# Kernel tuning notes

Hardware: AMD Instinct MI355X
Metric: run time of the kernel (lower is better)

Reference implementation:

```python
import jax, jax.numpy as jnp
import numpy as np

B, S, HID = 2, 2048, 2048
H, KVH, D = 32, 4, 128
EPS = 1e-6
ROPE_THETA = 1e6
INIT = 0.02


def setup_inputs() -> dict:
    key = jax.random.key(0)
    ks = jax.random.split(key, 6)
    hidden_states = jax.random.normal(ks[0], (B, S, HID), jnp.float32)
    q_w = jax.random.normal(ks[1], (HID, H * D), jnp.float32) * INIT
    k_w = jax.random.normal(ks[2], (HID, KVH * D), jnp.float32) * INIT
    v_w = jax.random.normal(ks[3], (HID, KVH * D), jnp.float32) * INIT
    o_w = jax.random.normal(ks[4], (H * D, HID), jnp.float32) * INIT
    q_norm_w = jnp.ones((D,), jnp.float32)
    k_norm_w = jnp.ones((D,), jnp.float32)
    # rotary embeddings, computed once per position (B, S, D)
    pos = jnp.arange(S, dtype=jnp.float32)
    inv_freq = 1.0 / (ROPE_THETA ** (jnp.arange(0, D, 2, dtype=jnp.float32) / D))
    freqs = pos[:, None] * inv_freq[None, :]          # (S, D/2)
    emb = jnp.concatenate([freqs, freqs], axis=-1)    # (S, D)
    cos = jnp.broadcast_to(jnp.cos(emb)[None], (B, S, D))
    sin = jnp.broadcast_to(jnp.sin(emb)[None], (B, S, D))
    # causal mask (is_causal=True, sliding_window=None)
    attn_mask = jnp.tril(jnp.ones((S, S), bool))[None, None]  # (1,1,S,S)
    return {"hidden_states": hidden_states, "cos": cos, "sin": sin,
            "q_w": q_w, "k_w": k_w, "v_w": v_w, "o_w": o_w,
            "q_norm_w": q_norm_w, "k_norm_w": k_norm_w, "attn_mask": attn_mask}


def _rms_norm(x, w):
    xf = x.astype(jnp.float32)
    var = jnp.mean(jax.lax.square(xf), axis=-1, keepdims=True)
    return (w * (xf * jax.lax.rsqrt(var + EPS))).astype(x.dtype)


def _rotate_half(x):
    x1, x2 = jnp.split(x, 2, axis=-1)
    return jnp.concatenate([-x2, x1], axis=-1)


def _apply_rope(q, k, cos, sin):
    # q: (B,H,S,D), k: (B,KVH,S,D); cos/sin: (B,S,D) -> (B,1,S,D)
    cos = cos[:, None]
    sin = sin[:, None]
    q = q * cos + _rotate_half(q) * sin
    k = k * cos + _rotate_half(k) * sin
    return q, k


def reference(hidden_states, cos, sin, q_w, k_w, v_w, o_w, q_norm_w, k_norm_w, attn_mask):
    b, s, _ = hidden_states.shape
    scaling = D ** (-0.5)
    # projections + per-head QK RMSNorm
    q = _rms_norm((hidden_states @ q_w).reshape(b, s, H, D), q_norm_w)
    k = _rms_norm((hidden_states @ k_w).reshape(b, s, KVH, D), k_norm_w)
    v = (hidden_states @ v_w).reshape(b, s, KVH, D)
    q = jnp.transpose(q, (0, 2, 1, 3))   # (b,H,s,D)
    k = jnp.transpose(k, (0, 2, 1, 3))   # (b,KVH,s,D)
    v = jnp.transpose(v, (0, 2, 1, 3))
    q, k = _apply_rope(q, k, cos, sin)
    # GQA: repeat KV heads across groups
    groups = H // KVH
    k = jnp.repeat(k, groups, axis=1)    # (b,H,s,D)
    v = jnp.repeat(v, groups, axis=1)
    # eager softmax attention (fp32 softmax)
    scores = jnp.einsum('bhqd,bhkd->bhqk', q, k).astype(jnp.float32) * scaling
    scores = jnp.where(attn_mask, scores, jnp.float32(-1e30))
    probs = jax.nn.softmax(scores, axis=-1).astype(q.dtype)
    attn = jnp.einsum('bhqk,bhkd->bhqd', probs, v)
    attn = jnp.transpose(attn, (0, 2, 1, 3)).reshape(b, s, H * D)
    return attn @ o_w
```

## Files before the change

### kernel.cpp

```cpp
#include <hip/hip_runtime.h>
#include <hip/hip_bf16.h>

typedef unsigned short u16;
typedef __attribute__((ext_vector_type(4))) float f32x4;
typedef __attribute__((ext_vector_type(16))) float f32x16;
typedef __attribute__((ext_vector_type(8))) short bf16x8;
typedef __attribute__((ext_vector_type(4))) unsigned u32x4;

#define B_ 2
#define S_ 2048
#define HID_ 2048
#define H_ 32
#define KVH_ 4
#define D_ 128
#define M_ 4096
#define NQ_ 4096
#define NKV_ 512

typedef const __attribute__((address_space(1))) void gconst_void;
typedef __attribute__((address_space(3))) void lds_void;

static __device__ __forceinline__ void gload_lds16(const void* g, void* l) {
  __builtin_amdgcn_global_load_lds((gconst_void*)g, (lds_void*)l, 16, 0, 0);
}

#define WAITV(N) asm volatile("s_waitcnt vmcnt(" #N ")" ::: "memory")
#define WAITL0() asm volatile("s_waitcnt lgkmcnt(0)" ::: "memory")
#define SBAR() __builtin_amdgcn_s_barrier()
#define SCHED0() __builtin_amdgcn_sched_barrier(0)
#define CFENCE() asm volatile("" ::: "memory")

static __device__ __forceinline__ u16 f2b(float f) {
  union { float f; unsigned i; } x; x.f = f;
  return (u16)((x.i + 0x7fffu + ((x.i >> 16) & 1u)) >> 16);
}
static __device__ __forceinline__ float b2f(u16 u) {
  union { unsigned i; float f; } x; x.i = ((unsigned)u) << 16;
  return x.f;
}
static __device__ __forceinline__ float max3f(float a, float b, float c) {
  float d;
  asm("v_max3_f32 %0, %1, %2, %3" : "=v"(d) : "v"(a), "v"(b), "v"(c));
  return d;
}

static __device__ __forceinline__ void tr_tile(const float* __restrict__ W,
    u16* __restrict__ Wt, int K, int N, int n0, int k0, u16 (*t)[72]) {
  int tid = threadIdx.x;
  int r = tid >> 4;
  int c4 = (tid & 15) * 4;
#pragma unroll
  for (int i = 0; i < 4; i++) {
    int k = r + i * 16;
    float4 v = *reinterpret_cast<const float4*>(W + (size_t)(k0 + k) * N + n0 + c4);
    t[k][c4 + 0] = f2b(v.x); t[k][c4 + 1] = f2b(v.y);
    t[k][c4 + 2] = f2b(v.z); t[k][c4 + 3] = f2b(v.w);
  }
  __syncthreads();
#pragma unroll
  for (int i = 0; i < 4; i++) {
    int n = r + i * 16;
    ushort4 o;
    o.x = t[c4 + 0][n]; o.y = t[c4 + 1][n]; o.z = t[c4 + 2][n]; o.w = t[c4 + 3][n];
    *reinterpret_cast<ushort4*>(Wt + (size_t)(n0 + n) * K + k0 + c4) = o;
  }
}

__global__ __launch_bounds__(256) void k_prep(const float* __restrict__ hidden, u16* __restrict__ hb,
    const float* __restrict__ qw, u16* __restrict__ qwt,
    const float* __restrict__ kw, u16* __restrict__ kwt,
    const float* __restrict__ vw, u16* __restrict__ vwt,
    const float* __restrict__ ow, u16* __restrict__ owt) {
  __shared__ u16 t[64][72];
  const int bid = blockIdx.x;
  if (bid < 2048) {
    const int n4 = M_ * HID_ / 4;
    int i = bid * 256 + threadIdx.x;
    const int stride = 2048 * 256;
    for (; i < n4; i += stride) {
      float4 v = reinterpret_cast<const float4*>(hidden)[i];
      ushort4 o;
      o.x = f2b(v.x); o.y = f2b(v.y); o.z = f2b(v.z); o.w = f2b(v.w);
      reinterpret_cast<ushort4*>(hb)[i] = o;
    }
  } else if (bid < 4096) {
    int l = bid - 2048;
    tr_tile(qw, qwt, HID_, NQ_, (l & 63) * 64, (l >> 6) * 64, t);
  } else if (bid < 4352) {
    int l = bid - 4096;
    tr_tile(kw, kwt, HID_, NKV_, (l & 7) * 64, (l >> 3) * 64, t);
  } else if (bid < 4608) {
    int l = bid - 4352;
    tr_tile(vw, vwt, HID_, NKV_, (l & 7) * 64, (l >> 3) * 64, t);
  } else {
    int l = bid - 4608;
    tr_tile(ow, owt, NQ_, HID_, (l & 31) * 64, (l >> 5) * 64, t);
  }
}

__device__ __forceinline__ void gemm_core(const u16* __restrict__ A, const u16* __restrict__ Bt,
                                          int K, int m0, int n0,
                                          u16* As, u16* Bs, f32x4 (&acc)[4][4]) {
  const int tid = threadIdx.x;
  const int lane = tid & 63;
  const int wid = tid >> 6;
  const int wr = wid >> 1, wc = wid & 1;
  const int lrow = lane & 15;
  const int hi = lane >> 4;
  const f32x4 zz = {0.f, 0.f, 0.f, 0.f};
#pragma unroll
  for (int i = 0; i < 4; i++)
#pragma unroll
    for (int j = 0; j < 4; j++) acc[i][j] = zz;

  const int srow = tid >> 3;
  const int sc16 = tid & 7;
  const int nk = K >> 6;
  int cur = 0;

#pragma unroll
  for (int rep = 0; rep < 4; rep++) {
    int row = rep * 32 + srow;
    int gcol = ((sc16 ^ (row & 7)) << 3);
    gload_lds16(A + (size_t)(m0 + row) * K + gcol, As + row * 64 + sc16 * 8);
    gload_lds16(Bt + (size_t)(n0 + row) * K + gcol, Bs + row * 64 + sc16 * 8);
  }

  for (int t = 0; t < nk; t++) {
    if (t + 1 < nk) {
      int nxt = cur ^ 1;
      int kb = (t + 1) << 6;
#pragma unroll
      for (int rep = 0; rep < 4; rep++) {
        int row = rep * 32 + srow;
        int gcol = kb + ((sc16 ^ (row & 7)) << 3);
        gload_lds16(A + (size_t)(m0 + row) * K + gcol, As + nxt * 8192 + row * 64 + sc16 * 8);
        gload_lds16(Bt + (size_t)(n0 + row) * K + gcol, Bs + nxt * 8192 + row * 64 + sc16 * 8);
      }
      WAITV(8);
    } else {
      WAITV(0);
    }
    SCHED0(); SBAR(); CFENCE(); SCHED0();

    const u16* Ac = As + cur * 8192;
    const u16* Bc = Bs + cur * 8192;
#pragma unroll
    for (int kc = 0; kc < 2; kc++) {
      bf16x8 af[4], bfr[4];
#pragma unroll
      for (int i = 0; i < 4; i++) {
        int row = wr * 64 + i * 16 + lrow;
        af[i] = *reinterpret_cast<const bf16x8*>(Ac + row * 64 + ((((kc << 2) + hi) ^ (row & 7)) << 3));
      }
#pragma unroll
      for (int j = 0; j < 4; j++) {
        int row = wc * 64 + j * 16 + lrow;
        bfr[j] = *reinterpret_cast<const bf16x8*>(Bc + row * 64 + ((((kc << 2) + hi) ^ (row & 7)) << 3));
      }
#pragma unroll
      for (int i = 0; i < 4; i++)
#pragma unroll
        for (int j = 0; j < 4; j++)
          acc[i][j] = __builtin_amdgcn_mfma_f32_16x16x32_bf16(af[i], bfr[j], acc[i][j], 0, 0, 0);
    }
    SBAR(); SCHED0();
    cur ^= 1;
  }
}

__global__ __launch_bounds__(512, 2) void k_gemm_q8(const u16* __restrict__ A,
    const u16* __restrict__ Bt, u16* __restrict__ qb) {
  __shared__ u16 Ash[2][2][128 * 64];
  __shared__ u16 Bsh[2][2][128 * 64];
  const int bid = blockIdx.x;
  const int wg = (bid & 7) * 32 + (bid >> 3);
  const int mt = wg & 15, nt = wg >> 4;
  const int m0 = mt * 256, n0 = nt * 256;
  const int K = HID_, nk = K >> 6;
  const int tid = threadIdx.x, lane = tid & 63;
  const int wv = tid >> 6, wr = wv >> 2, wc = wv & 3;
  const int lrow = lane & 15, hi4 = lane >> 4;

  const int s0r = tid >> 3, sc = tid & 7;
  const int s1r = (tid + 512) >> 3;

  auto stgA = [&](int h, int t, int d) {
    gload_lds16(A + (size_t)(m0 + h * 128 + s0r) * K + t * 64 + ((sc ^ (s0r & 7)) << 3),
                &Ash[d][h][s0r * 64 + sc * 8]);
    gload_lds16(A + (size_t)(m0 + h * 128 + s1r) * K + t * 64 + ((sc ^ (s1r & 7)) << 3),
                &Ash[d][h][s1r * 64 + sc * 8]);
  };
  auto stgB = [&](int h, int t, int d) {
    gload_lds16(Bt + (size_t)(n0 + h * 128 + s0r) * K + t * 64 + ((sc ^ (s0r & 7)) << 3),
                &Bsh[d][h][s0r * 64 + sc * 8]);
    gload_lds16(Bt + (size_t)(n0 + h * 128 + s1r) * K + t * 64 + ((sc ^ (s1r & 7)) << 3),
                &Bsh[d][h][s1r * 64 + sc * 8]);
  };

  f32x4 acc[8][4];
  const f32x4 zz = {0.f, 0.f, 0.f, 0.f};
#pragma unroll
  for (int f = 0; f < 8; f++)
#pragma unroll
    for (int j = 0; j < 4; j++) acc[f][j] = zz;

  bf16x8 af0[4][2], af1[4][2], bfr[2][2];

  auto lda = [&](bf16x8 (&dst)[4][2], int mh, int d) {
#pragma unroll
    for (int fi = 0; fi < 4; fi++) {
      int row = fi * 32 + wr * 16 + lrow;
#pragma unroll
      for (int kk = 0; kk < 2; kk++)
        dst[fi][kk] = *reinterpret_cast<const bf16x8*>(
            &Ash[d][mh][row * 64 + ((((kk << 2) + hi4) ^ (row & 7)) << 3)]);
    }
  };
  auto ldb = [&](int nh, int d) {
#pragma unroll
    for (int ji = 0; ji < 2; ji++) {
      int row = ji * 64 + wc * 16 + lrow;
#pragma unroll
      for (int kk = 0; kk < 2; kk++)
        bfr[ji][kk] = *reinterpret_cast<const bf16x8*>(
            &Bsh[d][nh][row * 64 + ((((kk << 2) + hi4) ^ (row & 7)) << 3)]);
    }
  };
  auto mq = [&](bf16x8 (&afh)[4][2], int mh, int nh) {
    __builtin_amdgcn_s_setprio(1);
#pragma unroll
    for (int kk = 0; kk < 2; kk++)
#pragma unroll
      for (int fi = 0; fi < 4; fi++)
#pragma unroll
        for (int ji = 0; ji < 2; ji++)
          acc[mh * 4 + fi][nh * 2 + ji] = __builtin_amdgcn_mfma_f32_16x16x32_bf16(
              afh[fi][kk], bfr[ji][kk], acc[mh * 4 + fi][nh * 2 + ji], 0, 0, 0);
    __builtin_amdgcn_s_setprio(0);
  };

  stgA(0, 0, 0); stgA(1, 0, 0); stgB(0, 0, 0); stgB(1, 0, 0);
  WAITV(2); SCHED0();
  SBAR(); SCHED0();

  for (int t = 0; t < nk; t++) {
    const int d = t & 1, nd = d ^ 1;
    const bool pre = (t + 1 < nk);
    lda(af0, 0, d); ldb(0, d);
    if (pre) stgA(0, t + 1, nd);
    SCHED0(); SBAR();
    WAITL0(); SCHED0();
    mq(af0, 0, 0);
    SBAR(); SCHED0();
    lda(af1, 1, d);
    if (pre) stgA(1, t + 1, nd);
    WAITV(4); SCHED0(); SBAR();
    WAITL0(); SCHED0();
    mq(af1, 1, 0);
    SBAR(); SCHED0();
    ldb(1, d);
    if (pre) stgB(0, t + 1, nd);
    SCHED0(); SBAR();
    WAITL0(); SCHED0();
    mq(af1, 1, 1);
    SBAR(); SCHED0();
    if (pre) stgB(1, t + 1, nd);
    WAITV(2); SCHED0(); SBAR();
    mq(af0, 0, 1);
    SBAR(); SCHED0();
  }

  const int lr4 = hi4 * 4, lc = lane & 15;
#pragma unroll
  for (int f = 0; f < 8; f++)
#pragma unroll
    for (int j = 0; j < 4; j++)
#pragma unroll
      for (int rr = 0; rr < 4; rr++) {
        int m = m0 + f * 32 + wr * 16 + lr4 + rr;
        int ncol = n0 + j * 64 + wc * 16 + lc;
        int b = m >> 11, s = m & (S_ - 1);
        int head = ncol >> 7, dd = ncol & 127;
        qb[(((size_t)b * H_ + head) * S_ + s) * D_ + dd] = f2b(acc[f][j][rr]);
      }
}

__global__ __launch_bounds__(256, 2) void k_gemm_kv(const u16* __restrict__ hb,
    const u16* __restrict__ kwt, const u16* __restrict__ vwt,
    u16* __restrict__ kb, u16* __restrict__ vb) {
  __shared__ u16 As[2 * 128 * 64], Bs[2 * 128 * 64];
  const int bid = blockIdx.x;
  const int wg = (bid & 7) * 32 + (bid >> 3);
  const int mt = wg & 31, nt = wg >> 5;
  const bool isv = nt >= 4;
  const int head = isv ? nt - 4 : nt;
  const u16* Bt = isv ? vwt : kwt;
  f32x4 acc[4][4];
  gemm_core(hb, Bt, HID_, mt * 128, head * 128, As, Bs, acc);
  const int lane = threadIdx.x & 63;
  const int wid = threadIdx.x >> 6;
  const int wr = wid >> 1, wc = wid & 1;
  const int lr4 = (lane >> 4) * 4, lc = lane & 15;
#pragma unroll
  for (int i = 0; i < 4; i++)
#pragma unroll
    for (int j = 0; j < 4; j++)
#pragma unroll
      for (int r = 0; r < 4; r++) {
        int m = mt * 128 + wr * 64 + i * 16 + lr4 + r;
        int d = wc * 64 + j * 16 + lc;
        int b = m >> 11, s = m & (S_ - 1);
        u16 val = f2b(acc[i][j][r]);
        if (isv) vb[(((size_t)b * KVH_ + head) * D_ + d) * S_ + s] = val;
        else     kb[(((size_t)b * KVH_ + head) * S_ + s) * D_ + d] = val;
      }
}

__global__ __launch_bounds__(512, 2) void k_gemm_o8(const u16* __restrict__ A,
    const u16* __restrict__ Bt, float* __restrict__ out) {
  __shared__ u16 Ash[2][2][128 * 64];
  __shared__ u16 Bsh[2][128 * 64];
  const int bid = blockIdx.x;
  const int wg = (bid & 7) * 32 + (bid >> 3);
  const int mt = wg & 15, nt = wg >> 4;
  const int m0 = mt * 256, n0 = nt * 128;
  const int K = NQ_, nk = K >> 6;
  const int tid = threadIdx.x, lane = tid & 63;
  const int wv = tid >> 6, wr = wv >> 2, wc = wv & 3;
  const int lrow = lane & 15, hi4 = lane >> 4;

  const int s0r = tid >> 3, sc = tid & 7;
  const int s1r = (tid + 512) >> 3;

  auto stgA = [&](int h, int t, int d) {
    gload_lds16(A + (size_t)(m0 + h * 128 + s0r) * K + t * 64 + ((sc ^ (s0r & 7)) << 3),
                &Ash[d][h][s0r * 64 + sc * 8]);
    gload_lds16(A + (size_t)(m0 + h * 128 + s1r) * K + t * 64 + ((sc ^ (s1r & 7)) << 3),
                &Ash[d][h][s1r * 64 + sc * 8]);
  };
  auto stgB = [&](int t, int d) {
    gload_lds16(Bt + (size_t)(n0 + s0r) * K + t * 64 + ((sc ^ (s0r & 7)) << 3),
                &Bsh[d][s0r * 64 + sc * 8]);
    gload_lds16(Bt + (size_t)(n0 + s1r) * K + t * 64 + ((sc ^ (s1r & 7)) << 3),
                &Bsh[d][s1r * 64 + sc * 8]);
  };

  f32x4 acc[8][2];
  const f32x4 zz = {0.f, 0.f, 0.f, 0.f};
#pragma unroll
  for (int f = 0; f < 8; f++) { acc[f][0] = zz; acc[f][1] = zz; }

  bf16x8 af0[4][2], af1[4][2], bfr[2][2];

  auto lda = [&](bf16x8 (&dst)[4][2], int mh, int d) {
#pragma unroll
    for (int fi = 0; fi < 4; fi++) {
      int row = fi * 32 + wr * 16 + lrow;
#pragma unroll
      for (int kk = 0; kk < 2; kk++)
        dst[fi][kk] = *reinterpret_cast<const bf16x8*>(
            &Ash[d][mh][row * 64 + ((((kk << 2) + hi4) ^ (row & 7)) << 3)]);
    }
  };
  auto ldb = [&](int d) {
#pragma unroll
    for (int ji = 0; ji < 2; ji++) {
      int row = ji * 64 + wc * 16 + lrow;
#pragma unroll
      for (int kk = 0; kk < 2; kk++)
        bfr[ji][kk] = *reinterpret_cast<const bf16x8*>(
            &Bsh[d][row * 64 + ((((kk << 2) + hi4) ^ (row & 7)) << 3)]);
    }
  };
  auto mq = [&](bf16x8 (&afh)[4][2], int mh) {
    __builtin_amdgcn_s_setprio(1);
#pragma unroll
    for (int kk = 0; kk < 2; kk++)
#pragma unroll
      for (int fi = 0; fi < 4; fi++)
#pragma unroll
        for (int ji = 0; ji < 2; ji++)
          acc[mh * 4 + fi][ji] = __builtin_amdgcn_mfma_f32_16x16x32_bf16(
              afh[fi][kk], bfr[ji][kk], acc[mh * 4 + fi][ji], 0, 0, 0);
    __builtin_amdgcn_s_setprio(0);
  };

  stgA(0, 0, 0); stgB(0, 0); stgA(1, 0, 0);
  WAITV(2); SCHED0();
  SBAR(); SCHED0();

  for (int t = 0; t < nk; t++) {
    const int d = t & 1, nd = d ^ 1;
    const bool pre = (t + 1 < nk);
    lda(af0, 0, d); ldb(d);
    if (pre) { stgA(0, t + 1, nd); WAITV(2); } else { WAITV(0); }
    SCHED0(); SBAR();
    WAITL0(); SCHED0();
    mq(af0, 0);
    SBAR(); SCHED0();
    lda(af1, 1, d);
    if (pre) { stgB(t + 1, nd); stgA(1, t + 1, nd); WAITV(4); }
    SCHED0(); SBAR();
    WAITL0(); SCHED0();
    mq(af1, 1);
    if (pre) WAITV(2);
    SCHED0(); SBAR(); SCHED0();
  }

  const int lr4 = hi4 * 4, lc = lane & 15;
#pragma unroll
  for (int f = 0; f < 8; f++)
#pragma unroll
    for (int j = 0; j < 2; j++)
#pragma unroll
      for (int rr = 0; rr < 4; rr++) {
        int m = m0 + f * 32 + wr * 16 + lr4 + rr;
        int n = n0 + j * 64 + wc * 16 + lc;
        out[(size_t)m * HID_ + n] = acc[f][j][rr];
      }
}

__global__ __launch_bounds__(256) void k_norm_rope(u16* __restrict__ qb, u16* __restrict__ kb,
    const float* __restrict__ cosp, const float* __restrict__ sinp,
    const float* __restrict__ qnw, const float* __restrict__ knw) {
  int row = blockIdx.x * 4 + (threadIdx.x >> 6);
  int lane = threadIdx.x & 63;
  const int QROWS = B_ * H_ * S_;
  u16* ptr; const float* nw; int b, s; float os;
  if (row < QROWS) {
    ptr = qb + (size_t)row * D_; nw = qnw;
    s = row & (S_ - 1); b = row / (H_ * S_);
    os = 0.08838834764831845f * 1.44269504088896340f;
  } else {
    int r2 = row - QROWS;
    ptr = kb + (size_t)r2 * D_; nw = knw;
    s = r2 & (S_ - 1); b = r2 / (KVH_ * S_);
    os = 1.0f;
  }
  int d = lane * 2;
  float x0 = b2f(ptr[d]), x1 = b2f(ptr[d + 1]);
  float ss = x0 * x0 + x1 * x1;
#pragma unroll
  for (int m = 1; m < 64; m <<= 1) ss += __shfl_xor(ss, m);
  float inv = rsqrtf(ss * (1.0f / 128.0f) + 1e-6f) * os;
  x0 = x0 * inv * nw[d]; x1 = x1 * inv * nw[d + 1];
  float p0 = __shfl_xor(x0, 32), p1 = __shfl_xor(x1, 32);
  float r0 = (lane < 32) ? -p0 : p0;
  float r1 = (lane < 32) ? -p1 : p1;
  const float* cp = cosp + ((size_t)b * S_ + s) * D_;
  const float* sp = sinp + ((size_t)b * S_ + s) * D_;
  ptr[d]     = f2b(x0 * cp[d]     + r0 * sp[d]);
  ptr[d + 1] = f2b(x1 * cp[d + 1] + r1 * sp[d + 1]);
}

__global__ __launch_bounds__(256, 2) void k_attn(const u16* __restrict__ q,
    const u16* __restrict__ k, const u16* __restrict__ vt, u16* __restrict__ out) {
  __shared__ u16 Kb[2 * 64 * 128];
  __shared__ u16 Vb[128 * 64];
  const int bid = blockIdx.x;
  const int wg = (bid & 7) * 128 + (bid >> 3);
  const int qt = 15 - (wg & 15);
  const int bh = wg >> 4;
  const int b = bh >> 5, h = bh & 31;
  const int kvh = h >> 3;
  const int tid = threadIdx.x, lane = tid & 63, w = tid >> 6;
  const int lq = lane & 31, hi = lane >> 5;
  const u16* qp  = q  + ((size_t)(b * H_ + h) * S_) * D_;
  const u16* kp  = k  + ((size_t)(b * KVH_ + kvh) * S_) * D_;
  const u16* vtp = vt + ((size_t)(b * KVH_ + kvh) * D_) * S_;

  const int rowKa = tid >> 4;
  const int colK  = ((tid & 15) ^ (rowKa & 15)) << 3;
  const int rowVa = tid >> 3;
  const int colV  = ((tid & 7) ^ (rowVa & 7)) << 3;

  auto stageK = [&](int n0, int cu) {
    u16* kd = Kb + cu * 8192 + tid * 8;
#pragma unroll
    for (int p = 0; p < 4; p++)
      gload_lds16(kp + (size_t)(n0 + p * 16 + rowKa) * D_ + colK, kd + p * 2048);
  };
  auto stageV = [&](int n0) {
    u16* vd = Vb + tid * 8;
#pragma unroll
    for (int p = 0; p < 4; p++)
      gload_lds16(vtp + (size_t)(p * 32 + rowVa) * S_ + n0 + colV, vd + p * 2048);
  };

  const f32x16 z16 = {0.f};
  const int q0 = qt * 128;
  const int last = 2 * qt + 1;
  const int qg = q0 + 32 * w + lq;
  int cur = 0;

  stageK(0, 0);
  stageV(0);

  bf16x8 qf[8];
#pragma unroll
  for (int ds = 0; ds < 8; ds++)
    qf[ds] = *reinterpret_cast<const bf16x8*>(qp + (size_t)qg * D_ + ds * 16 + hi * 8);

  f32x16 oacc[4];
#pragma unroll
  for (int dt = 0; dt < 4; dt++) oacc[dt] = z16;
  float mrun = -1e30f, lrun = 0.f;

  for (int nt = 0; nt <= last; nt++) {
    const int n0 = nt * 64;
    if (nt < last) {
      stageK(n0 + 64, cur ^ 1);
      WAITV(8);
    } else {
      WAITV(4);
    }
    SCHED0(); SBAR(); CFENCE(); SCHED0();

    const u16* Kc = Kb + cur * 8192;
    const bool skip = (n0 > q0 + 32 * w + 31);

    f32x16 sacc[2];
    if (!skip) {
      const bool needmask = (n0 + 63 > q0 + 32 * w);

      sacc[0] = z16; sacc[1] = z16;
#pragma unroll
      for (int ds = 0; ds < 8; ds++) {
        const int sl = (((ds << 1) + hi) ^ (lq & 15)) << 3;
        bf16x8 ka0 = *reinterpret_cast<const bf16x8*>(Kc + lq * 128 + sl);
        bf16x8 ka1 = *reinterpret_cast<const bf16x8*>(Kc + (lq + 32) * 128 + sl);
        __builtin_amdgcn_s_setprio(1);
        sacc[0] = __builtin_amdgcn_mfma_f32_32x32x16_bf16(ka0, qf[ds], sacc[0], 0, 0, 0);
        sacc[1] = __builtin_amdgcn_mfma_f32_32x32x16_bf16(ka1, qf[ds], sacc[1], 0, 0, 0);
        __builtin_amdgcn_s_setprio(0);
      }

      if (needmask) {
#pragma unroll
        for (int t = 0; t < 2; t++)
#pragma unroll
          for (int r = 0; r < 16; r++) {
            int kvg = n0 + 32 * t + (r & 3) + 8 * (r >> 2) + 4 * hi;
            if (kvg > qg) sacc[t][r] = -1e30f;
          }
      }
      float tm = fmaxf(sacc[0][0], sacc[0][1]);
#pragma unroll
      for (int i = 1; i < 16; i++) {
        const int e0 = 2 * i, e1 = 2 * i + 1;
        tm = max3f(tm, sacc[e0 >> 4][e0 & 15], sacc[e1 >> 4][e1 & 15]);
      }
      tm = fmaxf(tm, __shfl_xor(tm, 32));
      if (__any(tm > mrun + 8.f)) {
        float mn = fmaxf(mrun, tm);
        float al = exp2f(mrun - mn);
        mrun = mn;
        lrun *= al;
#pragma unroll
        for (int r = 0; r < 16; r++) {
          float ar = __shfl(al, (r & 3) + 8 * (r >> 2) + 4 * hi);
#pragma unroll
          for (int dt = 0; dt < 4; dt++) oacc[dt][r] *= ar;
        }
      }
      float rs = 0.f;
#pragma unroll
      for (int t = 0; t < 2; t++)
#pragma unroll
        for (int r = 0; r < 16; r++) {
          float pv = exp2f(sacc[t][r] - mrun);
          sacc[t][r] = pv;
          rs += pv;
        }
      rs += __shfl_xor(rs, 32);
      lrun += rs;
    }

    if (nt < last) WAITV(4); else WAITV(0);
    SCHED0(); SBAR(); CFENCE(); SCHED0();

    if (!skip) {
      u32x4 pa[4];
#pragma unroll
      for (int t = 0; t < 2; t++)
#pragma unroll
        for (int ksl = 0; ksl < 2; ksl++) {
          unsigned wa, wb, wc2, wd;
          asm("v_cvt_pk_bf16_f32 %0, %1, %2" : "=v"(wa)
              : "v"(sacc[t][8 * ksl + 0]), "v"(sacc[t][8 * ksl + 1]));
          asm("v_cvt_pk_bf16_f32 %0, %1, %2" : "=v"(wb)
              : "v"(sacc[t][8 * ksl + 2]), "v"(sacc[t][8 * ksl + 3]));
          asm("v_cvt_pk_bf16_f32 %0, %1, %2" : "=v"(wc2)
              : "v"(sacc[t][8 * ksl + 4]), "v"(sacc[t][8 * ksl + 5]));
          asm("v_cvt_pk_bf16_f32 %0, %1, %2" : "=v"(wd)
              : "v"(sacc[t][8 * ksl + 6]), "v"(sacc[t][8 * ksl + 7]));
          asm("v_permlane32_swap_b32 %0, %1" : "+v"(wa), "+v"(wc2));
          asm("v_permlane32_swap_b32 %0, %1" : "+v"(wb), "+v"(wd));
          u32x4 t4 = {wa, wb, wc2, wd};
          pa[t * 2 + ksl] = t4;
        }

#pragma unroll
      for (int ks = 0; ks < 4; ks++) {
        bf16x8 paf = __builtin_bit_cast(bf16x8, pa[ks]);
        bf16x8 bv[4];
#pragma unroll
        for (int dt = 0; dt < 4; dt++) {
          int rowv = dt * 32 + lq;
          bv[dt] = *reinterpret_cast<const bf16x8*>(
              Vb + rowv * 64 + ((((ks << 1) + hi) ^ (rowv & 7)) << 3));
        }
        __builtin_amdgcn_s_setprio(1);
#pragma unroll
        for (int dt = 0; dt < 4; dt++)
          oacc[dt] = __builtin_amdgcn_mfma_f32_32x32x16_bf16(paf, bv[dt], oacc[dt], 0, 0, 0);
        __builtin_amdgcn_s_setprio(0);
      }
    }

    if (nt < last) {
      SBAR(); SCHED0();
      stageV(nt * 64 + 64);
    }
    cur ^= 1;
  }

  float linv = 1.0f / lrun;
#pragma unroll
  for (int r = 0; r < 16; r++) {
    const int idx_r = (r & 3) + 8 * (r >> 2) + 4 * hi;
    float lr = __shfl(linv, idx_r);
    size_t base = ((size_t)b * S_ + (q0 + 32 * w + idx_r)) * NQ_ + h * D_ + lq;
#pragma unroll
    for (int dt = 0; dt < 4; dt++)
      out[base + dt * 32] = f2b(oacc[dt][r] * lr);
  }
}

extern "C" void kernel_launch(void* const* d_in, const int* in_sizes, int n_in,
                              void* d_out, int out_size, void* d_ws, size_t ws_size,
                              hipStream_t stream) {
  const float* hidden = (const float*)d_in[0];
  const float* cosp   = (const float*)d_in[1];
  const float* sinp   = (const float*)d_in[2];
  const float* q_w    = (const float*)d_in[3];
  const float* k_w    = (const float*)d_in[4];
  const float* v_w    = (const float*)d_in[5];
  const float* o_w    = (const float*)d_in[6];
  const float* qnw    = (const float*)d_in[7];
  const float* knw    = (const float*)d_in[8];

  char* p = (char*)d_ws;
  u16* hb  = (u16*)p; p += (size_t)M_ * HID_ * 2;
  u16* qwt = (u16*)p; p += (size_t)NQ_ * HID_ * 2;
  u16* kwt = (u16*)p; p += (size_t)NKV_ * HID_ * 2;
  u16* vwt = (u16*)p; p += (size_t)NKV_ * HID_ * 2;
  u16* owt = (u16*)p; p += (size_t)HID_ * NQ_ * 2;
  u16* qb  = (u16*)p; p += (size_t)B_ * H_ * S_ * D_ * 2;
  u16* kb  = (u16*)p; p += (size_t)B_ * KVH_ * S_ * D_ * 2;
  u16* vb  = (u16*)p; p += (size_t)B_ * KVH_ * S_ * D_ * 2;
  u16* ab  = (u16*)p; p += (size_t)M_ * NQ_ * 2;

  k_prep<<<6656, 256, 0, stream>>>(hidden, hb, q_w, qwt, k_w, kwt, v_w, vwt, o_w, owt);
  k_gemm_q8<<<256, 512, 0, stream>>>(hb, qwt, qb);
  k_gemm_kv<<<256, 256, 0, stream>>>(hb, kwt, vwt, kb, vb);
  k_norm_rope<<<(B_ * H_ * S_ + B_ * KVH_ * S_) / 4, 256, 0, stream>>>(qb, kb, cosp, sinp, qnw, knw);
  k_attn<<<1024, 256, 0, stream>>>(qb, kb, vb, ab);
  k_gemm_o8<<<256, 512, 0, stream>>>(ab, owt, (float*)d_out);
}
```

Baseline: 376.6 us.

## Split-K output GEMM with 256x256 tiles, pair causal attention tiles, vectorize norm-rope

```diff
diff --git a/kernel.cpp b/kernel.cpp
--- a/kernel.cpp
+++ b/kernel.cpp
@@ -286,6 +286,134 @@
       }
 }
 
+__global__ __launch_bounds__(512, 2) void k_gemm_o2(const u16* __restrict__ A,
+    const u16* __restrict__ Bt, float* __restrict__ out, float* __restrict__ part1) {
+  __shared__ u16 Ash[2][2][128 * 64];
+  __shared__ u16 Bsh[2][2][128 * 64];
+  const int bid = blockIdx.x;
+  const int wg = (bid & 7) * 32 + (bid >> 3);
+  const int ks = wg & 1, mt = (wg >> 1) & 15, nt = wg >> 5;
+  const int m0 = mt * 256, n0 = nt * 256;
+  const int kb0 = ks * 2048;
+  const int K = NQ_, nk = 32;
+  const int tid = threadIdx.x, lane = tid & 63;
+  const int wv = tid >> 6, wr = wv >> 2, wc = wv & 3;
+  const int lrow = lane & 15, hi4 = lane >> 4;
+
+  const int s0r = tid >> 3, sc = tid & 7;
+  const int s1r = (tid + 512) >> 3;
+
+  auto stgA = [&](int h, int t, int d) {
+    gload_lds16(A + (size_t)(m0 + h * 128 + s0r) * K + kb0 + t * 64 + ((sc ^ (s0r & 7)) << 3),
+                &Ash[d][h][s0r * 64 + sc * 8]);
+    gload_lds16(A + (size_t)(m0 + h * 128 + s1r) * K + kb0 + t * 64 + ((sc ^ (s1r & 7)) << 3),
+                &Ash[d][h][s1r * 64 + sc * 8]);
+  };
+  auto stgB = [&](int h, int t, int d) {
+    gload_lds16(Bt + (size_t)(n0 + h * 128 + s0r) * K + kb0 + t * 64 + ((sc ^ (s0r & 7)) << 3),
+                &Bsh[d][h][s0r * 64 + sc * 8]);
+    gload_lds16(Bt + (size_t)(n0 + h * 128 + s1r) * K + kb0 + t * 64 + ((sc ^ (s1r & 7)) << 3),
+                &Bsh[d][h][s1r * 64 + sc * 8]);
+  };
+
+  f32x4 acc[8][4];
+  const f32x4 zz = {0.f, 0.f, 0.f, 0.f};
+#pragma unroll
+  for (int f = 0; f < 8; f++)
+#pragma unroll
+    for (int j = 0; j < 4; j++) acc[f][j] = zz;
+
+  bf16x8 af0[4][2], af1[4][2], bfr[2][2];
+
+  auto lda = [&](bf16x8 (&dst)[4][2], int mh, int d) {
+#pragma unroll
+    for (int fi = 0; fi < 4; fi++) {
+      int row = fi * 32 + wr * 16 + lrow;
+#pragma unroll
+      for (int kk = 0; kk < 2; kk++)
+        dst[fi][kk] = *reinterpret_cast<const bf16x8*>(
+            &Ash[d][mh][row * 64 + ((((kk << 2) + hi4) ^ (row & 7)) << 3)]);
+    }
+  };
+  auto ldb = [&](int nh, int d) {
+#pragma unroll
+    for (int ji = 0; ji < 2; ji++) {
+      int row = ji * 64 + wc * 16 + lrow;
+#pragma unroll
+      for (int kk = 0; kk < 2; kk++)
+        bfr[ji][kk] = *reinterpret_cast<const bf16x8*>(
+            &Bsh[d][nh][row * 64 + ((((kk << 2) + hi4) ^ (row & 7)) << 3)]);
+    }
+  };
+  auto mq = [&](bf16x8 (&afh)[4][2], int mh, int nh) {
+    __builtin_amdgcn_s_setprio(1);
+#pragma unroll
+    for (int kk = 0; kk < 2; kk++)
+#pragma unroll
+      for (int fi = 0; fi < 4; fi++)
+#pragma unroll
+        for (int ji = 0; ji < 2; ji++)
+          acc[mh * 4 + fi][nh * 2 + ji] = __builtin_amdgcn_mfma_f32_16x16x32_bf16(
+              afh[fi][kk], bfr[ji][kk], acc[mh * 4 + fi][nh * 2 + ji], 0, 0, 0);
+    __builtin_amdgcn_s_setprio(0);
+  };
+
+  stgA(0, 0, 0); stgA(1, 0, 0); stgB(0, 0, 0); stgB(1, 0, 0);
+  WAITV(2); SCHED0();
+  SBAR(); SCHED0();
+
+  for (int t = 0; t < nk; t++) {
+    const int d = t & 1, nd = d ^ 1;
+    const bool pre = (t + 1 < nk);
+    lda(af0, 0, d); ldb(0, d);
+    if (pre) stgA(0, t + 1, nd);
+    SCHED0(); SBAR();
+    WAITL0(); SCHED0();
+    mq(af0, 0, 0);
+    SBAR(); SCHED0();
+    lda(af1, 1, d);
+    if (pre) stgA(1, t + 1, nd);
+    WAITV(4); SCHED0(); SBAR();
+    WAITL0(); SCHED0();
+    mq(af1, 1, 0);
+    SBAR(); SCHED0();
+    ldb(1, d);
+    if (pre) stgB(0, t + 1, nd);
+    SCHED0(); SBAR();
+    WAITL0(); SCHED0();
+    mq(af1, 1, 1);
+    SBAR(); SCHED0();
+    if (pre) stgB(1, t + 1, nd);
+    WAITV(2); SCHED0(); SBAR();
+    mq(af0, 0, 1);
+    SBAR(); SCHED0();
+  }
+
+  float* dst = ks ? part1 : out;
+  const int lr4 = hi4 * 4, lc = lane & 15;
+#pragma unroll
+  for (int f = 0; f < 8; f++)
+#pragma unroll
+    for (int j = 0; j < 4; j++)
+#pragma unroll
+      for (int rr = 0; rr < 4; rr++) {
+        int m = m0 + f * 32 + wr * 16 + lr4 + rr;
+        int n = n0 + j * 64 + wc * 16 + lc;
+        dst[(size_t)m * HID_ + n] = acc[f][j][rr];
+      }
+}
+
+__global__ void k_osum(float* __restrict__ out, const float* __restrict__ part1, int n4) {
+  int i = blockIdx.x * blockDim.x + threadIdx.x;
+  const int stride = gridDim.x * blockDim.x;
+  for (; i < n4; i += stride) {
+    float4 a = reinterpret_cast<float4*>(out)[i];
+    float4 b = reinterpret_cast<const float4*>(part1)[i];
+    a.x += b.x; a.y += b.y; a.z += b.z; a.w += b.w;
+    reinterpret_cast<float4*>(out)[i] = a;
+  }
+}
+
 __global__ __launch_bounds__(256, 2) void k_gemm_kv(const u16* __restrict__ hb,
     const u16* __restrict__ kwt, const u16* __restrict__ vwt,
     u16* __restrict__ kb, u16* __restrict__ vb) {
@@ -317,110 +445,6 @@
       }
 }
 
-__global__ __launch_bounds__(512, 2) void k_gemm_o8(const u16* __restrict__ A,
-    const u16* __restrict__ Bt, float* __restrict__ out) {
-  __shared__ u16 Ash[2][2][128 * 64];
-  __shared__ u16 Bsh[2][128 * 64];
-  const int bid = blockIdx.x;
-  const int wg = (bid & 7) * 32 + (bid >> 3);
-  const int mt = wg & 15, nt = wg >> 4;
-  const int m0 = mt * 256, n0 = nt * 128;
-  const int K = NQ_, nk = K >> 6;
-  const int tid = threadIdx.x, lane = tid & 63;
-  const int wv = tid >> 6, wr = wv >> 2, wc = wv & 3;
-  const int lrow = lane & 15, hi4 = lane >> 4;
-
-  const int s0r = tid >> 3, sc = tid & 7;
-  const int s1r = (tid + 512) >> 3;
-
-  auto stgA = [&](int h, int t, int d) {
-    gload_lds16(A + (size_t)(m0 + h * 128 + s0r) * K + t * 64 + ((sc ^ (s0r & 7)) << 3),
-                &Ash[d][h][s0r * 64 + sc * 8]);
-    gload_lds16(A + (size_t)(m0 + h * 128 + s1r) * K + t * 64 + ((sc ^ (s1r & 7)) << 3),
-                &Ash[d][h][s1r * 64 + sc * 8]);
-  };
-  auto stgB = [&](int t, int d) {
-    gload_lds16(Bt + (size_t)(n0 + s0r) * K + t * 64 + ((sc ^ (s0r & 7)) << 3),
-                &Bsh[d][s0r * 64 + sc * 8]);
-    gload_lds16(Bt + (size_t)(n0 + s1r) * K + t * 64 + ((sc ^ (s1r & 7)) << 3),
-                &Bsh[d][s1r * 64 + sc * 8]);
-  };
-
-  f32x4 acc[8][2];
-  const f32x4 zz = {0.f, 0.f, 0.f, 0.f};
-#pragma unroll
-  for (int f = 0; f < 8; f++) { acc[f][0] = zz; acc[f][1] = zz; }
-
-  bf16x8 af0[4][2], af1[4][2], bfr[2][2];
-
-  auto lda = [&](bf16x8 (&dst)[4][2], int mh, int d) {
-#pragma unroll
-    for (int fi = 0; fi < 4; fi++) {
-      int row = fi * 32 + wr * 16 + lrow;
-#pragma unroll
-      for (int kk = 0; kk < 2; kk++)
-        dst[fi][kk] = *reinterpret_cast<const bf16x8*>(
-            &Ash[d][mh][row * 64 + ((((kk << 2) + hi4) ^ (row & 7)) << 3)]);
-    }
-  };
-  auto ldb = [&](int d) {
-#pragma unroll
-    for (int ji = 0; ji < 2; ji++) {
-      int row = ji * 64 + wc * 16 + lrow;
-#pragma unroll
-      for (int kk = 0; kk < 2; kk++)
-        bfr[ji][kk] = *reinterpret_cast<const bf16x8*>(
-            &Bsh[d][row * 64 + ((((kk << 2) + hi4) ^ (row & 7)) << 3)]);
-    }
-  };
-  auto mq = [&](bf16x8 (&afh)[4][2], int mh) {
-    __builtin_amdgcn_s_setprio(1);
-#pragma unroll
-    for (int kk = 0; kk < 2; kk++)
-#pragma unroll
-      for (int fi = 0; fi < 4; fi++)
-#pragma unroll
-        for (int ji = 0; ji < 2; ji++)
-          acc[mh * 4 + fi][ji] = __builtin_amdgcn_mfma_f32_16x16x32_bf16(
-              afh[fi][kk], bfr[ji][kk], acc[mh * 4 + fi][ji], 0, 0, 0);
-    __builtin_amdgcn_s_setprio(0);
-  };
-
-  stgA(0, 0, 0); stgB(0, 0); stgA(1, 0, 0);
-  WAITV(2); SCHED0();
-  SBAR(); SCHED0();
-
-  for (int t = 0; t < nk; t++) {
-    const int d = t & 1, nd = d ^ 1;
-    const bool pre = (t + 1 < nk);
-    lda(af0, 0, d); ldb(d);
-    if (pre) { stgA(0, t + 1, nd); WAITV(2); } else { WAITV(0); }
-    SCHED0(); SBAR();
-    WAITL0(); SCHED0();
-    mq(af0, 0);
-    SBAR(); SCHED0();
-    lda(af1, 1, d);
-    if (pre) { stgB(t + 1, nd); stgA(1, t + 1, nd); WAITV(4); }
-    SCHED0(); SBAR();
-    WAITL0(); SCHED0();
-    mq(af1, 1);
-    if (pre) WAITV(2);
-    SCHED0(); SBAR(); SCHED0();
-  }
-
-  const int lr4 = hi4 * 4, lc = lane & 15;
-#pragma unroll
-  for (int f = 0; f < 8; f++)
-#pragma unroll
-    for (int j = 0; j < 2; j++)
-#pragma unroll
-      for (int rr = 0; rr < 4; rr++) {
-        int m = m0 + f * 32 + wr * 16 + lr4 + rr;
-        int n = n0 + j * 64 + wc * 16 + lc;
-        out[(size_t)m * HID_ + n] = acc[f][j][rr];
-      }
-}
-
 __global__ __launch_bounds__(256) void k_norm_rope(u16* __restrict__ qb, u16* __restrict__ kb,
     const float* __restrict__ cosp, const float* __restrict__ sinp,
     const float* __restrict__ qnw, const float* __restrict__ knw) {
@@ -439,19 +463,22 @@
     os = 1.0f;
   }
   int d = lane * 2;
-  float x0 = b2f(ptr[d]), x1 = b2f(ptr[d + 1]);
+  unsigned xw = *reinterpret_cast<const unsigned*>(ptr + d);
+  float x0 = b2f((u16)(xw & 0xffffu)), x1 = b2f((u16)(xw >> 16));
   float ss = x0 * x0 + x1 * x1;
 #pragma unroll
   for (int m = 1; m < 64; m <<= 1) ss += __shfl_xor(ss, m);
   float inv = rsqrtf(ss * (1.0f / 128.0f) + 1e-6f) * os;
-  x0 = x0 * inv * nw[d]; x1 = x1 * inv * nw[d + 1];
+  float2 nwv = *reinterpret_cast<const float2*>(nw + d);
+  x0 = x0 * inv * nwv.x; x1 = x1 * inv * nwv.y;
   float p0 = __shfl_xor(x0, 32), p1 = __shfl_xor(x1, 32);
   float r0 = (lane < 32) ? -p0 : p0;
   float r1 = (lane < 32) ? -p1 : p1;
-  const float* cp = cosp + ((size_t)b * S_ + s) * D_;
-  const float* sp = sinp + ((size_t)b * S_ + s) * D_;
-  ptr[d]     = f2b(x0 * cp[d]     + r0 * sp[d]);
-  ptr[d + 1] = f2b(x1 * cp[d + 1] + r1 * sp[d + 1]);
+  float2 cv = *reinterpret_cast<const float2*>(cosp + ((size_t)b * S_ + s) * D_ + d);
+  float2 sv = *reinterpret_cast<const float2*>(sinp + ((size_t)b * S_ + s) * D_ + d);
+  u16 o0 = f2b(x0 * cv.x + r0 * sv.x);
+  u16 o1 = f2b(x1 * cv.y + r1 * sv.y);
+  *reinterpret_cast<unsigned*>(ptr + d) = ((unsigned)o1 << 16) | o0;
 }
 
 __global__ __launch_bounds__(256, 2) void k_attn(const u16* __restrict__ q,
@@ -459,9 +486,8 @@
   __shared__ u16 Kb[2 * 64 * 128];
   __shared__ u16 Vb[128 * 64];
   const int bid = blockIdx.x;
-  const int wg = (bid & 7) * 128 + (bid >> 3);
-  const int qt = 15 - (wg & 15);
-  const int bh = wg >> 4;
+  const int wg = (bid & 7) * 64 + (bid >> 3);
+  const int qx = wg & 7, bh = wg >> 3;
   const int b = bh >> 5, h = bh & 31;
   const int kvh = h >> 3;
   const int tid = threadIdx.x, lane = tid & 63, w = tid >> 6;
@@ -489,152 +515,157 @@
   };
 
   const f32x16 z16 = {0.f};
-  const int q0 = qt * 128;
-  const int last = 2 * qt + 1;
-  const int qg = q0 + 32 * w + lq;
   int cur = 0;
 
-  stageK(0, 0);
-  stageV(0);
-
-  bf16x8 qf[8];
-#pragma unroll
-  for (int ds = 0; ds < 8; ds++)
-    qf[ds] = *reinterpret_cast<const bf16x8*>(qp + (size_t)qg * D_ + ds * 16 + hi * 8);
-
-  f32x16 oacc[4];
-#pragma unroll
-  for (int dt = 0; dt < 4; dt++) oacc[dt] = z16;
-  float mrun = -1e30f, lrun = 0.f;
-
-  for (int nt = 0; nt <= last; nt++) {
-    const int n0 = nt * 64;
-    if (nt < last) {
-      stageK(n0 + 64, cur ^ 1);
-      WAITV(8);
-    } else {
-      WAITV(4);
-    }
-    SCHED0(); SBAR(); CFENCE(); SCHED0();
-
-    const u16* Kc = Kb + cur * 8192;
-    const bool skip = (n0 > q0 + 32 * w + 31);
-
-    f32x16 sacc[2];
-    if (!skip) {
-      const bool needmask = (n0 + 63 > q0 + 32 * w);
-
-      sacc[0] = z16; sacc[1] = z16;
-#pragma unroll
-      for (int ds = 0; ds < 8; ds++) {
-        const int sl = (((ds << 1) + hi) ^ (lq & 15)) << 3;
-        bf16x8 ka0 = *reinterpret_cast<const bf16x8*>(Kc + lq * 128 + sl);
-        bf16x8 ka1 = *reinterpret_cast<const bf16x8*>(Kc + (lq + 32) * 128 + sl);
-        __builtin_amdgcn_s_setprio(1);
-        sacc[0] = __builtin_amdgcn_mfma_f32_32x32x16_bf16(ka0, qf[ds], sacc[0], 0, 0, 0);
-        sacc[1] = __builtin_amdgcn_mfma_f32_32x32x16_bf16(ka1, qf[ds], sacc[1], 0, 0, 0);
-        __builtin_amdgcn_s_setprio(0);
-      }
-
-      if (needmask) {
+  for (int half = 0; half < 2; half++) {
+    const int qt = half ? (15 - qx) : qx;
+    const int q0 = qt * 128;
+    const int last = 2 * qt + 1;
+    const int qg = q0 + 32 * w + lq;
+
+    SBAR(); SCHED0();
+    stageK(0, cur);
+    stageV(0);
+
+    bf16x8 qf[8];
+#pragma unroll
+    for (int ds = 0; ds < 8; ds++)
+      qf[ds] = *reinterpret_cast<const bf16x8*>(qp + (size_t)qg * D_ + ds * 16 + hi * 8);
+
+    f32x16 oacc[4];
+#pragma unroll
+    for (int dt = 0; dt < 4; dt++) oacc[dt] = z16;
+    float mrun = -1e30f, lrun = 0.f;
+
+    for (int nt = 0; nt <= last; nt++) {
+      const int n0 = nt * 64;
+      if (nt < last) {
+        stageK(n0 + 64, cur ^ 1);
+        WAITV(8);
+      } else {
+        WAITV(4);
+      }
+      SCHED0(); SBAR(); CFENCE(); SCHED0();
+
+      const u16* Kc = Kb + cur * 8192;
+      const bool skip = (n0 > q0 + 32 * w + 31);
+
+      f32x16 sacc[2];
+      if (!skip) {
+        const bool needmask = (n0 + 63 > q0 + 32 * w);
+
+        sacc[0] = z16; sacc[1] = z16;
+#pragma unroll
+        for (int ds = 0; ds < 8; ds++) {
+          const int sl = (((ds << 1) + hi) ^ (lq & 15)) << 3;
+          bf16x8 ka0 = *reinterpret_cast<const bf16x8*>(Kc + lq * 128 + sl);
+          bf16x8 ka1 = *reinterpret_cast<const bf16x8*>(Kc + (lq + 32) * 128 + sl);
+          __builtin_amdgcn_s_setprio(1);
+          sacc[0] = __builtin_amdgcn_mfma_f32_32x32x16_bf16(ka0, qf[ds], sacc[0], 0, 0, 0);
+          sacc[1] = __builtin_amdgcn_mfma_f32_32x32x16_bf16(ka1, qf[ds], sacc[1], 0, 0, 0);
+          __builtin_amdgcn_s_setprio(0);
+        }
+
+        if (needmask) {
+#pragma unroll
+          for (int t = 0; t < 2; t++)
+#pragma unroll
+            for (int r = 0; r < 16; r++) {
+              int kvg = n0 + 32 * t + (r & 3) + 8 * (r >> 2) + 4 * hi;
+              if (kvg > qg) sacc[t][r] = -1e30f;
+            }
+        }
+        float tm = fmaxf(sacc[0][0], sacc[0][1]);
+#pragma unroll
+        for (int i = 1; i < 16; i++) {
+          const int e0 = 2 * i, e1 = 2 * i + 1;
+          tm = max3f(tm, sacc[e0 >> 4][e0 & 15], sacc[e1 >> 4][e1 & 15]);
+        }
+        tm = fmaxf(tm, __shfl_xor(tm, 32));
+        if (__any(tm > mrun + 8.f)) {
+          float mn = fmaxf(mrun, tm);
+          float al = exp2f(mrun - mn);
+          mrun = mn;
+          lrun *= al;
+#pragma unroll
+          for (int r = 0; r < 16; r++) {
+            float ar = __shfl(al, (r & 3) + 8 * (r >> 2) + 4 * hi);
+#pragma unroll
+            for (int dt = 0; dt < 4; dt++) oacc[dt][r] *= ar;
+          }
+        }
+        float rs = 0.f;
 #pragma unroll
         for (int t = 0; t < 2; t++)
 #pragma unroll
           for (int r = 0; r < 16; r++) {
-            int kvg = n0 + 32 * t + (r & 3) + 8 * (r >> 2) + 4 * hi;
-            if (kvg > qg) sacc[t][r] = -1e30f;
+            float pv = exp2f(sacc[t][r] - mrun);
+            sacc[t][r] = pv;
+            rs += pv;
           }
-      }
-      float tm = fmaxf(sacc[0][0], sacc[0][1]);
-#pragma unroll
-      for (int i = 1; i < 16; i++) {
-        const int e0 = 2 * i, e1 = 2 * i + 1;
-        tm = max3f(tm, sacc[e0 >> 4][e0 & 15], sacc[e1 >> 4][e1 & 15]);
-      }
-      tm = fmaxf(tm, __shfl_xor(tm, 32));
-      if (__any(tm > mrun + 8.f)) {
-        float mn = fmaxf(mrun, tm);
-        float al = exp2f(mrun - mn);
-        mrun = mn;
-        lrun *= al;
-#pragma unroll
-        for (int r = 0; r < 16; r++) {
-          float ar = __shfl(al, (r & 3) + 8 * (r >> 2) + 4 * hi);
-#pragma unroll
-          for (int dt = 0; dt < 4; dt++) oacc[dt][r] *= ar;
+        rs += __shfl_xor(rs, 32);
+        lrun += rs;
+      }
+
+      if (nt < last) WAITV(4); else WAITV(0);
+      SCHED0(); SBAR(); CFENCE(); SCHED0();
+
+      if (!skip) {
+        u32x4 pa[4];
+#pragma unroll
+        for (int t = 0; t < 2; t++)
+#pragma unroll
+          for (int ksl = 0; ksl < 2; ksl++) {
+            unsigned wa, wb, wc2, wd;
+            asm("v_cvt_pk_bf16_f32 %0, %1, %2" : "=v"(wa)
+                : "v"(sacc[t][8 * ksl + 0]), "v"(sacc[t][8 * ksl + 1]));
+            asm("v_cvt_pk_bf16_f32 %0, %1, %2" : "=v"(wb)
+                : "v"(sacc[t][8 * ksl + 2]), "v"(sacc[t][8 * ksl + 3]));
+            asm("v_cvt_pk_bf16_f32 %0, %1, %2" : "=v"(wc2)
+                : "v"(sacc[t][8 * ksl + 4]), "v"(sacc[t][8 * ksl + 5]));
+            asm("v_cvt_pk_bf16_f32 %0, %1, %2" : "=v"(wd)
+                : "v"(sacc[t][8 * ksl + 6]), "v"(sacc[t][8 * ksl + 7]));
+            asm("v_permlane32_swap_b32 %0, %1" : "+v"(wa), "+v"(wc2));
+            asm("v_permlane32_swap_b32 %0, %1" : "+v"(wb), "+v"(wd));
+            u32x4 t4 = {wa, wb, wc2, wd};
+            pa[t * 2 + ksl] = t4;
+          }
+
+#pragma unroll
+        for (int ks = 0; ks < 4; ks++) {
+          bf16x8 paf = __builtin_bit_cast(bf16x8, pa[ks]);
+          bf16x8 bv[4];
+#pragma unroll
+          for (int dt = 0; dt < 4; dt++) {
+            int rowv = dt * 32 + lq;
+            bv[dt] = *reinterpret_cast<const bf16x8*>(
+                Vb + rowv * 64 + ((((ks << 1) + hi) ^ (rowv & 7)) << 3));
+          }
+          __builtin_amdgcn_s_setprio(1);
+#pragma unroll
+          for (int dt = 0; dt < 4; dt++)
+            oacc[dt] = __builtin_amdgcn_mfma_f32_32x32x16_bf16(paf, bv[dt], oacc[dt], 0, 0, 0);
+          __builtin_amdgcn_s_setprio(0);
         }
       }
-      float rs = 0.f;
-#pragma unroll
-      for (int t = 0; t < 2; t++)
-#pragma unroll
-        for (int r = 0; r < 16; r++) {
-          float pv = exp2f(sacc[t][r] - mrun);
-          sacc[t][r] = pv;
-          rs += pv;
-        }
-      rs += __shfl_xor(rs, 32);
-      lrun += rs;
-    }
-
-    if (nt < last) WAITV(4); else WAITV(0);
-    SCHED0(); SBAR(); CFENCE(); SCHED0();
-
-    if (!skip) {
-      u32x4 pa[4];
-#pragma unroll
-      for (int t = 0; t < 2; t++)
-#pragma unroll
-        for (int ksl = 0; ksl < 2; ksl++) {
-          unsigned wa, wb, wc2, wd;
-          asm("v_cvt_pk_bf16_f32 %0, %1, %2" : "=v"(wa)
-              : "v"(sacc[t][8 * ksl + 0]), "v"(sacc[t][8 * ksl + 1]));
-          asm("v_cvt_pk_bf16_f32 %0, %1, %2" : "=v"(wb)
-              : "v"(sacc[t][8 * ksl + 2]), "v"(sacc[t][8 * ksl + 3]));
-          asm("v_cvt_pk_bf16_f32 %0, %1, %2" : "=v"(wc2)
-              : "v"(sacc[t][8 * ksl + 4]), "v"(sacc[t][8 * ksl + 5]));
-          asm("v_cvt_pk_bf16_f32 %0, %1, %2" : "=v"(wd)
-              : "v"(sacc[t][8 * ksl + 6]), "v"(sacc[t][8 * ksl + 7]));
-          asm("v_permlane32_swap_b32 %0, %1" : "+v"(wa), "+v"(wc2));
-          asm("v_permlane32_swap_b32 %0, %1" : "+v"(wb), "+v"(wd));
-          u32x4 t4 = {wa, wb, wc2, wd};
-          pa[t * 2 + ksl] = t4;
-        }
-
-#pragma unroll
-      for (int ks = 0; ks < 4; ks++) {
-        bf16x8 paf = __builtin_bit_cast(bf16x8, pa[ks]);
-        bf16x8 bv[4];
-#pragma unroll
-        for (int dt = 0; dt < 4; dt++) {
-          int rowv = dt * 32 + lq;
-          bv[dt] = *reinterpret_cast<const bf16x8*>(
-              Vb + rowv * 64 + ((((ks << 1) + hi) ^ (rowv & 7)) << 3));
-        }
-        __builtin_amdgcn_s_setprio(1);
-#pragma unroll
-        for (int dt = 0; dt < 4; dt++)
-          oacc[dt] = __builtin_amdgcn_mfma_f32_32x32x16_bf16(paf, bv[dt], oacc[dt], 0, 0, 0);
-        __builtin_amdgcn_s_setprio(0);
-      }
-    }
-
-    if (nt < last) {
-      SBAR(); SCHED0();
-      stageV(nt * 64 + 64);
-    }
-    cur ^= 1;
-  }
-
-  float linv = 1.0f / lrun;
-#pragma unroll
-  for (int r = 0; r < 16; r++) {
-    const int idx_r = (r & 3) + 8 * (r >> 2) + 4 * hi;
-    float lr = __shfl(linv, idx_r);
-    size_t base = ((size_t)b * S_ + (q0 + 32 * w + idx_r)) * NQ_ + h * D_ + lq;
-#pragma unroll
-    for (int dt = 0; dt < 4; dt++)
-      out[base + dt * 32] = f2b(oacc[dt][r] * lr);
+
+      if (nt < last) {
+        SBAR(); SCHED0();
+        stageV(nt * 64 + 64);
+      }
+      cur ^= 1;
+    }
+
+    float linv = 1.0f / lrun;
+#pragma unroll
+    for (int r = 0; r < 16; r++) {
+      const int idx_r = (r & 3) + 8 * (r >> 2) + 4 * hi;
+      float lr = __shfl(linv, idx_r);
+      size_t base = ((size_t)b * S_ + (q0 + 32 * w + idx_r)) * NQ_ + h * D_ + lq;
+#pragma unroll
+      for (int dt = 0; dt < 4; dt++)
+        out[base + dt * 32] = f2b(oacc[dt][r] * lr);
+    }
   }
 }
 
@@ -662,10 +693,13 @@
   u16* vb  = (u16*)p; p += (size_t)B_ * KVH_ * S_ * D_ * 2;
   u16* ab  = (u16*)p; p += (size_t)M_ * NQ_ * 2;
 
+  float* part1 = (float*)hb;
+
   k_prep<<<6656, 256, 0, stream>>>(hidden, hb, q_w, qwt, k_w, kwt, v_w, vwt, o_w, owt);
   k_gemm_q8<<<256, 512, 0, stream>>>(hb, qwt, qb);
   k_gemm_kv<<<256, 256, 0, stream>>>(hb, kwt, vwt, kb, vb);
   k_norm_rope<<<(B_ * H_ * S_ + B_ * KVH_ * S_) / 4, 256, 0, stream>>>(qb, kb, cosp, sinp, qnw, knw);
-  k_attn<<<1024, 256, 0, stream>>>(qb, kb, vb, ab);
-  k_gemm_o8<<<256, 512, 0, stream>>>(ab, owt, (float*)d_out);
-}
+  k_attn<<<512, 256, 0, stream>>>(qb, kb, vb, ab);
+  k_gemm_o2<<<256, 512, 0, stream>>>(ab, owt, (float*)d_out, part1);
+  k_osum<<<2048, 256, 0, stream>>>((float*)d_out, part1, M_ * HID_ / 4);
+}
```

After: 338.1 us. 1.11x faster.
